# Optimization experiments

Hardware: AMD Instinct MI355X
Metric: run time of the kernel (lower is better)

## Reference

```python
import jax, jax.numpy as jnp
import numpy as np

B, T, E, H, L, V = 4, 1024, 768, 12, 6, 32000
HS = E // H
FF = 4 * E


def setup_inputs() -> dict:
    key = jax.random.key(0)
    ks = jax.random.split(key, 12)
    std = 0.02
    n = lambda k, shp: jax.random.normal(k, shp, jnp.float32) * std
    # sinusoidal position table (buffer, matches _get_pos_embed_table)
    pos = np.arange(T)[:, None].astype(np.float32)
    div = np.exp(np.arange(0, E, 2).astype(np.float32) * (-np.log(10000.0) / E))
    pet = np.zeros((T, E), np.float32)
    pet[:, 0::2] = np.sin(pos * div)
    pet[:, 1::2] = np.cos(pos * div)
    return {
        'tokens': jax.random.randint(ks[0], (B, T), 0, V),
        'targets': jax.random.randint(ks[1], (B, T), 0, V),
        'tok_emb': n(ks[2], (V, E)),
        'pet': jnp.asarray(pet),
        'wq': n(ks[3], (L, H, E, HS)),
        'wk': n(ks[4], (L, H, E, HS)),
        'wv': n(ks[5], (L, H, E, HS)),
        'w_proj': n(ks[6], (L, E, E)),
        'b_proj': jnp.zeros((L, E), jnp.float32),
        'ln1_g': jnp.ones((L, E), jnp.float32),
        'ln1_b': jnp.zeros((L, E), jnp.float32),
        'ln2_g': jnp.ones((L, E), jnp.float32),
        'ln2_b': jnp.zeros((L, E), jnp.float32),
        'w_ff1': n(ks[7], (L, E, FF)),
        'b_ff1': jnp.zeros((L, FF), jnp.float32),
        'w_ff2': n(ks[8], (L, FF, E)),
        'b_ff2': jnp.zeros((L, E), jnp.float32),
        'lnf_g': jnp.ones((E,), jnp.float32),
        'lnf_b': jnp.zeros((E,), jnp.float32),
        'w_out': n(ks[9], (E, V)),
        'b_out': jnp.zeros((V,), jnp.float32),
    }


def _ln(x, g, b, eps=1e-5):
    m = x.mean(-1, keepdims=True)
    v = ((x - m) ** 2).mean(-1, keepdims=True)
    return (x - m) / jnp.sqrt(v + eps) * g + b


def reference(tokens, targets, tok_emb, pet, wq, wk, wv, w_proj, b_proj,
              ln1_g, ln1_b, ln2_g, ln2_b, w_ff1, b_ff1, w_ff2, b_ff2,
              lnf_g, lnf_b, w_out, b_out):
    Tq = tokens.shape[1]
    x = tok_emb[tokens] + pet[:Tq]  # [B,T,E] (dropout=0 -> identity)
    mask = jnp.tril(jnp.ones((Tq, Tq), bool))
    for l in range(L):
        h = _ln(x, ln1_g[l], ln1_b[l])
        q = jnp.einsum('bte,hef->bhtf', h, wq[l])
        k = jnp.einsum('bte,hef->bhtf', h, wk[l])
        v = jnp.einsum('bte,hef->bhtf', h, wv[l])
        s = jnp.einsum('bhtf,bhsf->bhts', q, k) * (HS ** -0.5)
        s = jnp.where(mask, s, -jnp.inf)
        w = jax.nn.softmax(s, axis=-1)
        att = jnp.einsum('bhts,bhsf->bhtf', w, v)
        att = att.transpose(0, 2, 1, 3).reshape(x.shape[0], Tq, E)  # concat heads
        x = x + att @ w_proj[l] + b_proj[l]
        h2 = _ln(x, ln2_g[l], ln2_b[l])
        x = x + jax.nn.relu(h2 @ w_ff1[l] + b_ff1[l]) @ w_ff2[l] + b_ff2[l]
    x = _ln(x, lnf_g, lnf_b)
    logits = (x @ w_out + b_out).reshape(-1, V)  # [B*T, V]
    logp = jax.nn.log_softmax(logits, axis=-1)
    tgt = targets.reshape(-1)
    loss = -jnp.take_along_axis(logp, tgt[:, None], axis=1).mean()
    return logits, loss
```

## Files before the change

kernel.cpp:

```cpp
#include <hip/hip_runtime.h>
#include <math.h>

namespace {

constexpr int Bc = 4, Tc = 1024, Ec = 768, Hc = 12, Lc = 6;
constexpr int Vc = 32000, FFc = 3072, Mc = Bc * Tc;
constexpr int QKVN = 3 * Ec;

typedef __bf16 bf16x8 __attribute__((ext_vector_type(8)));
typedef float f32x4 __attribute__((ext_vector_type(4)));

__device__ __forceinline__ unsigned short f2bf(float f) {
  unsigned u = __builtin_bit_cast(unsigned, f);
  u += 0x7FFFu + ((u >> 16) & 1u);
  return (unsigned short)(u >> 16);
}

__device__ __forceinline__ float wave_sum(float v) {
#pragma unroll
  for (int off = 32; off > 0; off >>= 1) v += __shfl_xor(v, off, 64);
  return v;
}
__device__ __forceinline__ float block_sum256(float v, volatile float* red) {
  v = wave_sum(v);
  __syncthreads();
  if ((threadIdx.x & 63) == 0) red[threadIdx.x >> 6] = v;
  __syncthreads();
  return red[0] + red[1] + red[2] + red[3];
}
__device__ __forceinline__ void raw_barrier() {
  asm volatile("" ::: "memory");
  __builtin_amdgcn_s_barrier();
  asm volatile("" ::: "memory");
}

__global__ __launch_bounds__(256) void embed_k(const int* __restrict__ tokens,
                                               const float* __restrict__ emb,
                                               const float* __restrict__ pet,
                                               float* __restrict__ x) {
  int i = blockIdx.x * 256 + threadIdx.x;
  int m = i / Ec, e = i - m * Ec;
  int tok = tokens[m];
  x[i] = emb[(size_t)tok * Ec + e] + pet[(size_t)(m & (Tc - 1)) * Ec + e];
}

__global__ __launch_bounds__(256) void ln_k(const float* __restrict__ in,
                                            const float* __restrict__ g,
                                            const float* __restrict__ bb,
                                            unsigned short* __restrict__ outp) {
  __shared__ float red[4];
  int row = blockIdx.x, tid = threadIdx.x;
  const float* xr = in + (size_t)row * Ec;
  float v0 = xr[tid], v1 = xr[tid + 256], v2 = xr[tid + 512];
  float mean = block_sum256(v0 + v1 + v2, red) * (1.0f / 768.0f);
  float d0 = v0 - mean, d1 = v1 - mean, d2 = v2 - mean;
  float var = block_sum256(d0 * d0 + d1 * d1 + d2 * d2, red) * (1.0f / 768.0f);
  float rs = rsqrtf(var + 1e-5f);
  unsigned short* orow = outp + (size_t)row * Ec;
  orow[tid]       = f2bf(d0 * rs * g[tid]       + bb[tid]);
  orow[tid + 256] = f2bf(d1 * rs * g[tid + 256] + bb[tid + 256]);
  orow[tid + 512] = f2bf(d2 * rs * g[tid + 512] + bb[tid + 512]);
}

__global__ __launch_bounds__(256) void tcvt_k(const float* __restrict__ src,
                                              unsigned short* __restrict__ dst,
                                              int K, int N,
                                              size_t srcBatch, size_t dstBatch) {
  __shared__ float t[64][65];
  const float* s = src + blockIdx.z * srcBatch;
  unsigned short* d = dst + blockIdx.z * dstBatch;
  int k0 = blockIdx.y * 64, n0 = blockIdx.x * 64;
  int tid = threadIdx.x;
#pragma unroll
  for (int i = 0; i < 16; ++i) {
    int rr = (tid >> 6) + i * 4, cc = tid & 63;
    t[rr][cc] = s[(size_t)(k0 + rr) * N + n0 + cc];
  }
  __syncthreads();
#pragma unroll
  for (int i = 0; i < 16; ++i) {
    int rr = (tid >> 6) + i * 4, cc = tid & 63;
    d[(size_t)(n0 + rr) * K + k0 + cc] = f2bf(t[cc][rr]);
  }
}

__global__ __launch_bounds__(256) void qcvt_k(const float* __restrict__ wq,
                                              const float* __restrict__ wk,
                                              const float* __restrict__ wv,
                                              unsigned short* __restrict__ dst) {
  __shared__ float t[64][65];
  const int which = blockIdx.y / (Lc * Hc);
  const int z = blockIdx.y % (Lc * Hc), l = z / Hc, h = z % Hc;
  const float* src = which == 0 ? wq : (which == 1 ? wk : wv);
  const int k0 = blockIdx.x * 64;
  const int tid = threadIdx.x;
  const float* s = src + ((size_t)z * Ec + k0) * 64;
  unsigned short* d =
      dst + (size_t)l * QKVN * Ec + ((size_t)which * Ec + h * 64) * Ec + k0;
#pragma unroll
  for (int i = 0; i < 16; ++i) {
    int rr = (tid >> 6) + i * 4, cc = tid & 63;
    t[rr][cc] = s[(size_t)rr * 64 + cc];
  }
  __syncthreads();
#pragma unroll
  for (int i = 0; i < 16; ++i) {
    int rr = (tid >> 6) + i * 4, cc = tid & 63;
    d[(size_t)rr * Ec + cc] = f2bf(t[cc][rr]);
  }
}

#define GLDS16(g, l)                                              \
  __builtin_amdgcn_global_load_lds(                               \
      (const __attribute__((address_space(1))) void*)(g),         \
      (__attribute__((address_space(3))) void*)(l), 16, 0, 0)

template <int MODE, int BSRC, int BM, int BN, int GX>
__global__ __launch_bounds__(256) void mgemm_k(
    const unsigned short* __restrict__ A, const void* __restrict__ Bv,
    const float* __restrict__ bias, void* __restrict__ Cv,
    int M, int N, int K) {
  constexpr int MI = BM / 32, NF = BN / 32;
  constexpr int TL = BM / 32 + BN / 32;
  __shared__ unsigned short AsU[2][BM * 64];
  __shared__ unsigned short BsU[2][BN * 64];
  const int tid = threadIdx.x, lane = tid & 63, wave = tid >> 6;
  int bm, bn;
  if constexpr (GX == 1) {
    bm = blockIdx.y * BM;
    bn = blockIdx.x * BN;
  } else {
    bm = (blockIdx.z * GX + blockIdx.x) * BM;
    bn = blockIdx.y * BN;
  }
  const int wm = (wave >> 1) * (BM / 2), wn = (wave & 1) * (BN / 2);
  const int fr = lane & 15, fq = lane >> 4;
  const int lr8 = lane >> 3, lc8 = (lane & 7) * 8;
  const int sc8 = ((lane & 7) ^ (lr8 & 7)) * 8;
  f32x4 acc[MI][NF];
#pragma unroll
  for (int i = 0; i < MI; ++i)
#pragma unroll
    for (int j = 0; j < NF; ++j) acc[i][j] = (f32x4){0.f, 0.f, 0.f, 0.f};

  auto stage = [&](int k0, int pb) {
    {
      const unsigned short* g =
          A + (size_t)(bm + wave * (BM / 4) + lr8) * K + k0 + sc8;
      unsigned short* l = &AsU[pb][(wave * (BM / 4) + lr8) * 64 + lc8];
#pragma unroll
      for (int it = 0; it < BM / 32; ++it)
        GLDS16(g + (size_t)(it * 8) * K, l + it * 8 * 64);
    }
    if constexpr (BSRC == 0) {
      const unsigned short* Bt = (const unsigned short*)Bv;
      const unsigned short* g =
          Bt + (size_t)(bn + wave * (BN / 4) + lr8) * K + k0 + sc8;
      unsigned short* l = &BsU[pb][(wave * (BN / 4) + lr8) * 64 + lc8];
#pragma unroll
      for (int it = 0; it < BN / 32; ++it)
        GLDS16(g + (size_t)(it * 8) * K, l + it * 8 * 64);
    } else {
      const float* Bf = (const float*)Bv;
#pragma unroll
      for (int i = 0; i < 8; ++i) {
        int f4 = i * 256 + tid;
        int kk = f4 >> 5, c4 = (f4 & 31) * 4;
        float4 v = *(const float4*)(Bf + (size_t)(k0 + kk) * N + bn + c4);
        BsU[pb][(c4 + 0) * 64 + kk] = f2bf(v.x);
        BsU[pb][(c4 + 1) * 64 + kk] = f2bf(v.y);
        BsU[pb][(c4 + 2) * 64 + kk] = f2bf(v.z);
        BsU[pb][(c4 + 3) * 64 + kk] = f2bf(v.w);
      }
    }
  };

  auto compute = [&](int pb) {
#pragma unroll
    for (int kk = 0; kk < 2; ++kk) {
      bf16x8 af[MI], bfr[NF];
#pragma unroll
      for (int i = 0; i < MI; ++i) {
        int row = wm + i * 16 + fr;
        af[i] = *(const bf16x8*)((char*)AsU[pb] + row * 128 +
                                 ((kk * 64 + fq * 16) ^ ((row & 7) << 4)));
      }
#pragma unroll
      for (int j = 0; j < NF; ++j) {
        int row = wn + j * 16 + fr;
        if constexpr (BSRC == 0)
          bfr[j] = *(const bf16x8*)((char*)BsU[pb] + row * 128 +
                                    ((kk * 64 + fq * 16) ^ ((row & 7) << 4)));
        else
          bfr[j] = *(const bf16x8*)&BsU[pb][row * 64 + kk * 32 + fq * 8];
      }
#pragma unroll
      for (int i = 0; i < MI; ++i)
#pragma unroll
        for (int j = 0; j < NF; ++j)
          acc[i][j] = __builtin_amdgcn_mfma_f32_16x16x32_bf16(af[i], bfr[j],
                                                              acc[i][j], 0, 0, 0);
    }
  };

  const int nk = K >> 6;
  if constexpr (BSRC == 0) {
    stage(0, 0);
    for (int t = 0; t < nk; ++t) {
      const int pb = t & 1;
      if (t + 1 < nk) {
        stage((t + 1) << 6, pb ^ 1);
        if constexpr (TL == 8)      asm volatile("s_waitcnt vmcnt(8)" ::: "memory");
        else if constexpr (TL == 6) asm volatile("s_waitcnt vmcnt(6)" ::: "memory");
        else                        asm volatile("s_waitcnt vmcnt(4)" ::: "memory");
      } else {
        asm volatile("s_waitcnt vmcnt(0)" ::: "memory");
      }
      raw_barrier();
      compute(pb);
      raw_barrier();
    }
  } else {
    stage(0, 0);
    __syncthreads();
    for (int t = 0; t < nk; ++t) {
      const int pb = t & 1;
      if (t + 1 < nk) stage((t + 1) << 6, pb ^ 1);
      compute(pb);
      __syncthreads();
    }
  }
#pragma unroll
  for (int i = 0; i < MI; ++i) {
    int row0 = bm + wm + i * 16 + fq * 4;
#pragma unroll
    for (int j = 0; j < NF; ++j) {
      int col = bn + wn + j * 16 + fr;
      float bval = 0.f;
      if constexpr (MODE != 0) bval = bias[col];
#pragma unroll
      for (int r = 0; r < 4; ++r) {
        size_t idx = (size_t)(row0 + r) * N + col;
        float v = acc[i][j][r];
        if constexpr (MODE == 0) {
          ((unsigned short*)Cv)[idx] = f2bf(v);
        } else if constexpr (MODE == 1) {
          ((unsigned short*)Cv)[idx] = f2bf(fmaxf(v + bval, 0.f));
        } else if constexpr (MODE == 2) {
          float* C = (float*)Cv;
          C[idx] = C[idx] + v + bval;
        } else {
          ((float*)Cv)[idx] = v + bval;
        }
      }
    }
  }
}

__global__ __launch_bounds__(256) void fattn2_k(const unsigned short* __restrict__ qkv,
                                                unsigned short* __restrict__ att) {
  __shared__ unsigned short Ks[2][64 * 64];
  __shared__ unsigned short Vt[2][80 * 64];
  __shared__ unsigned short Pb[4][16 * 72];
  const int bh = blockIdx.y;
  const int b = bh / Hc, h = bh % Hc;
  const int qb = gridDim.x - 1 - blockIdx.x;
  const int q0 = qb * 128;
  const int tid = threadIdx.x, lane = tid & 63, w = tid >> 6;
  const int fr = lane & 15, fq = lane >> 4;
  const size_t base = (size_t)b * Tc * QKVN + h * 64;
  const int r0 = tid >> 3, c0 = (tid & 7) * 8;
  const int s2 = (tid & 31) * 2, c0v = (tid >> 5) * 8;
  const float SC = 0.125f * 1.44269504f;

  bf16x8 aq[2][2];
#pragma unroll
  for (int mi = 0; mi < 2; ++mi) {
    const unsigned short* qp =
        qkv + base + (size_t)(q0 + w * 32 + mi * 16 + fr) * QKVN + fq * 8;
    aq[mi][0] = *(const bf16x8*)qp;
    aq[mi][1] = *(const bf16x8*)(qp + 32);
  }
  f32x4 o[2][5];
  float m_run[2][4];
#pragma unroll
  for (int mi = 0; mi < 2; ++mi)
#pragma unroll
    for (int n = 0; n < 5; ++n) o[mi][n] = (f32x4){0.f, 0.f, 0.f, 0.f};
#pragma unroll
  for (int mi = 0; mi < 2; ++mi)
#pragma unroll
    for (int r = 0; r < 4; ++r) m_run[mi][r] = -INFINITY;

  {
#pragma unroll
    for (int bx = 0; bx < 2; ++bx) {
      unsigned* vt32 = (unsigned*)(Vt[bx] + 64 * 64);
      vt32[tid] = (tid < 32) ? 0x3F803F80u : 0u;
      vt32[tid + 256] = 0u;
    }
  }

  const int nt = 2 * qb + 2;
  uint4 pk0, pk1, pv0, pv1;
  auto loadt = [&](int s0) {
    const unsigned short* kg = qkv + base + Ec + (size_t)(s0 + r0) * QKVN + c0;
    pk0 = *(const uint4*)kg;
    pk1 = *(const uint4*)(kg + (size_t)32 * QKVN);
    const unsigned short* vg =
        qkv + base + 2 * Ec + (size_t)(s0 + s2) * QKVN + c0v;
    pv0 = *(const uint4*)vg;
    pv1 = *(const uint4*)(vg + QKVN);
  };
  auto writet = [&](int bx) {
    *(uint4*)((char*)Ks[bx] + (r0 * 128 + ((c0 * 2) ^ ((r0 & 7) << 4)))) = pk0;
    const int r1 = r0 + 32;
    *(uint4*)((char*)Ks[bx] + (r1 * 128 + ((c0 * 2) ^ ((r1 & 7) << 4)))) = pk1;
    const unsigned short* p0 = (const unsigned short*)&pv0;
    const unsigned short* p1 = (const unsigned short*)&pv1;
#pragma unroll
    for (int j = 0; j < 8; ++j) {
      int hs = c0v + j;
      unsigned pk = (unsigned)p0[j] | ((unsigned)p1[j] << 16);
      *(unsigned*)((char*)Vt[bx] + (hs * 128 + ((s2 * 2) ^ ((hs & 7) << 4)))) = pk;
    }
  };

  loadt(0);
  writet(0);
  __syncthreads();

  for (int it = 0; it < nt; ++it) {
    const int s0 = it * 64;
    const int pb = it & 1;
    if (it + 1 < nt) loadt(s0 + 64);

    f32x4 s[2][4];
#pragma unroll
    for (int mi = 0; mi < 2; ++mi)
#pragma unroll
      for (int n = 0; n < 4; ++n) s[mi][n] = (f32x4){0.f, 0.f, 0.f, 0.f};
    __builtin_amdgcn_s_setprio(1);
#pragma unroll
    for (int ss = 0; ss < 2; ++ss)
#pragma unroll
      for (int n = 0; n < 4; ++n) {
        int row = n * 16 + fr;
        bf16x8 kb = *(const bf16x8*)(
            (char*)Ks[pb] + (row * 128 + ((ss * 64 + fq * 16) ^ ((row & 7) << 4))));
#pragma unroll
        for (int mi = 0; mi < 2; ++mi)
          s[mi][n] = __builtin_amdgcn_mfma_f32_16x16x32_bf16(aq[mi][ss], kb,
                                                             s[mi][n], 0, 0, 0);
      }
    __builtin_amdgcn_s_setprio(0);

#pragma unroll
    for (int mi = 0; mi < 2; ++mi) {
      const int qlo = q0 + w * 32 + mi * 16;
      const bool need_mask = (s0 + 63 > qlo);
#pragma unroll
      for (int n = 0; n < 4; ++n) {
        int scol = s0 + n * 16 + fr;
#pragma unroll
        for (int r = 0; r < 4; ++r) {
          float v = s[mi][n][r] * SC;
          if (need_mask && scol > qlo + fq * 4 + r) v = -INFINITY;
          s[mi][n][r] = v;
        }
      }
      float mt[4];
#pragma unroll
      for (int r = 0; r < 4; ++r)
        mt[r] = fmaxf(fmaxf(s[mi][0][r], s[mi][1][r]),
                      fmaxf(s[mi][2][r], s[mi][3][r]));
#pragma unroll
      for (int off = 1; off <= 8; off <<= 1)
#pragma unroll
        for (int r = 0; r < 4; ++r)
          mt[r] = fmaxf(mt[r], __shfl_xor(mt[r], off, 64));
      bool csm = (mt[0] <= m_run[mi][0] + 8.f) & (mt[1] <= m_run[mi][1] + 8.f) &
                 (mt[2] <= m_run[mi][2] + 8.f) & (mt[3] <= m_run[mi][3] + 8.f);
      if (!__all(csm)) {
        float alpha[4];
#pragma unroll
        for (int r = 0; r < 4; ++r) {
          float mn = fmaxf(m_run[mi][r], mt[r]);
          alpha[r] = exp2f(m_run[mi][r] - mn);
          m_run[mi][r] = mn;
        }
#pragma unroll
        for (int n = 0; n < 5; ++n)
#pragma unroll
          for (int r = 0; r < 4; ++r) o[mi][n][r] *= alpha[r];
      }
#pragma unroll
      for (int n = 0; n < 4; ++n)
#pragma unroll
        for (int r = 0; r < 4; ++r)
          Pb[w][(fq * 4 + r) * 72 + n * 16 + fr] =
              f2bf(exp2f(s[mi][n][r] - m_run[mi][r]));
      __builtin_amdgcn_s_setprio(1);
#pragma unroll
      for (int ss = 0; ss < 2; ++ss) {
        bf16x8 pa = *(const bf16x8*)&Pb[w][fr * 72 + ss * 32 + fq * 8];
#pragma unroll
        for (int n = 0; n < 5; ++n) {
          int row = n * 16 + fr;
          bf16x8 vb = *(const bf16x8*)(
              (char*)Vt[pb] + (row * 128 + ((ss * 64 + fq * 16) ^ ((row & 7) << 4))));
          o[mi][n] = __builtin_amdgcn_mfma_f32_16x16x32_bf16(pa, vb, o[mi][n],
                                                             0, 0, 0);
        }
      }
      __builtin_amdgcn_s_setprio(0);
    }

    if (it + 1 < nt) writet(pb ^ 1);
    __syncthreads();
  }
#pragma unroll
  for (int mi = 0; mi < 2; ++mi)
#pragma unroll
    for (int r = 0; r < 4; ++r) {
      const float l = __shfl(o[mi][4][r], lane & 48, 64);
      const float inv = 1.0f / l;
      const int qrow = q0 + w * 32 + mi * 16 + fq * 4 + r;
      unsigned short* orow = att + ((size_t)(b * Tc + qrow)) * Ec + h * 64;
#pragma unroll
      for (int n = 0; n < 4; ++n) orow[n * 16 + fr] = f2bf(o[mi][n][r] * inv);
    }
}

__global__ __launch_bounds__(256) void loss_k(const float* __restrict__ logits,
                                              const int* __restrict__ targets,
                                              float* __restrict__ rowloss) {
  __shared__ float redm[4], reds[4];
  const int row = blockIdx.x, tid = threadIdx.x;
  const f32x4* lr4 = (const f32x4*)(logits + (size_t)row * Vc);
  float m = -INFINITY, s = 0.f;
  for (int j = tid; j < Vc / 4; j += 256) {
    f32x4 v = __builtin_nontemporal_load(lr4 + j);
    float m0 = fmaxf(fmaxf(v[0], v[1]), fmaxf(v[2], v[3]));
    float nm = fmaxf(m, m0);
    s = s * __expf(m - nm) + __expf(v[0] - nm) + __expf(v[1] - nm) +
        __expf(v[2] - nm) + __expf(v[3] - nm);
    m = nm;
  }
#pragma unroll
  for (int off = 32; off; off >>= 1) {
    float om = __shfl_xor(m, off, 64), os = __shfl_xor(s, off, 64);
    float nm = fmaxf(m, om);
    s = s * __expf(m - nm) + os * __expf(om - nm);
    m = nm;
  }
  if ((tid & 63) == 0) { redm[tid >> 6] = m; reds[tid >> 6] = s; }
  __syncthreads();
  if (tid == 0) {
    float M2 = redm[0], S2 = reds[0];
#pragma unroll
    for (int w = 1; w < 4; ++w) {
      float om = redm[w], os = reds[w];
      float nm = fmaxf(M2, om);
      S2 = S2 * __expf(M2 - nm) + os * __expf(om - nm);
      M2 = nm;
    }
    float lt = logits[(size_t)row * Vc + targets[row]];
    rowloss[row] = -(lt - M2 - logf(S2));
  }
}

__global__ __launch_bounds__(1024) void lossred_k(const float* __restrict__ rowloss,
                                                  float* __restrict__ outp) {
  __shared__ float red[16];
  float s = 0.f;
  for (int i = threadIdx.x; i < Mc; i += 1024) s += rowloss[i];
  s = wave_sum(s);
  if ((threadIdx.x & 63) == 0) red[threadIdx.x >> 6] = s;
  __syncthreads();
  if (threadIdx.x == 0) {
    float tot = 0.f;
#pragma unroll
    for (int i = 0; i < 16; ++i) tot += red[i];
    outp[0] = tot * (1.0f / (float)Mc);
  }
}

}

extern "C" void kernel_launch(void* const* d_in, const int* in_sizes, int n_in,
                              void* d_out, int out_size, void* d_ws, size_t ws_size,
                              hipStream_t stream) {
  const int*   tokens  = (const int*)d_in[0];
  const int*   targets = (const int*)d_in[1];
  const float* tok_emb = (const float*)d_in[2];
  const float* pet     = (const float*)d_in[3];
  const float* wq      = (const float*)d_in[4];
  const float* wk      = (const float*)d_in[5];
  const float* wv      = (const float*)d_in[6];
  const float* w_proj  = (const float*)d_in[7];
  const float* b_proj  = (const float*)d_in[8];
  const float* ln1_g   = (const float*)d_in[9];
  const float* ln1_b   = (const float*)d_in[10];
  const float* ln2_g   = (const float*)d_in[11];
  const float* ln2_b   = (const float*)d_in[12];
  const float* w_ff1   = (const float*)d_in[13];
  const float* b_ff1   = (const float*)d_in[14];
  const float* w_ff2   = (const float*)d_in[15];
  const float* b_ff2   = (const float*)d_in[16];
  const float* lnf_g   = (const float*)d_in[17];
  const float* lnf_b   = (const float*)d_in[18];
  const float* w_out   = (const float*)d_in[19];
  const float* b_out   = (const float*)d_in[20];

  float* out = (float*)d_out;
  char* ob = (char*)d_out;
  unsigned short* qkvA  = (unsigned short*)(ob + 0);
  unsigned short* attA  = (unsigned short*)(ob + 18874368);
  unsigned short* ffhA  = (unsigned short*)(ob + 25165824);
  unsigned short* qkvT  = (unsigned short*)(ob + 50331648);
  unsigned short* projT = (unsigned short*)(ob + 71565312);
  unsigned short* ff1T  = (unsigned short*)(ob + 78643200);
  unsigned short* ff2T  = (unsigned short*)(ob + 106954752);
  char* wb = (char*)d_ws;
  float* x = (float*)wb;
  unsigned short* hbuf = (unsigned short*)(wb + 12582912);
  float* rowloss = (float*)(wb + 18874368);
  unsigned short* woutT = (unsigned short*)(wb + 18890752);
  const bool wfit = ws_size >= (size_t)18890752 + 49152000;

  qcvt_k<<<dim3(12, 3 * Lc * Hc), 256, 0, stream>>>(wq, wk, wv, qkvT);
  tcvt_k<<<dim3(12, 12, 6), 256, 0, stream>>>(w_proj, projT, 768, 768,
                                              (size_t)589824, (size_t)589824);
  tcvt_k<<<dim3(48, 12, 6), 256, 0, stream>>>(w_ff1, ff1T, 768, 3072,
                                              (size_t)768 * 3072, (size_t)768 * 3072);
  tcvt_k<<<dim3(12, 48, 6), 256, 0, stream>>>(w_ff2, ff2T, 3072, 768,
                                              (size_t)768 * 3072, (size_t)768 * 3072);
  if (wfit)
    tcvt_k<<<dim3(500, 12, 1), 256, 0, stream>>>(w_out, woutT, 768, 32000, 0, 0);

  embed_k<<<(Mc * Ec) / 256, 256, 0, stream>>>(tokens, tok_emb, pet, x);

  for (int l = 0; l < Lc; ++l) {
    ln_k<<<Mc, 256, 0, stream>>>(x, ln1_g + (size_t)l * Ec, ln1_b + (size_t)l * Ec, hbuf);
    mgemm_k<0, 0, 128, 64, 1><<<dim3(36, 32), 256, 0, stream>>>(
        hbuf, qkvT + (size_t)l * QKVN * Ec, nullptr, qkvA, Mc, QKVN, Ec);
    fattn2_k<<<dim3(Tc / 128, Bc * Hc), 256, 0, stream>>>(qkvA, attA);
    mgemm_k<2, 0, 64, 64, 1><<<dim3(12, 64), 256, 0, stream>>>(
        attA, projT + (size_t)l * Ec * Ec, b_proj + (size_t)l * Ec, x, Mc, Ec, Ec);
    ln_k<<<Mc, 256, 0, stream>>>(x, ln2_g + (size_t)l * Ec, ln2_b + (size_t)l * Ec, hbuf);
    mgemm_k<1, 0, 128, 64, 1><<<dim3(48, 32), 256, 0, stream>>>(
        hbuf, ff1T + (size_t)l * Ec * FFc, b_ff1 + (size_t)l * FFc, ffhA, Mc, FFc, Ec);
    mgemm_k<2, 0, 64, 64, 1><<<dim3(12, 64), 256, 0, stream>>>(
        ffhA, ff2T + (size_t)l * Ec * FFc, b_ff2 + (size_t)l * Ec, x, Mc, Ec, FFc);
  }
  ln_k<<<Mc, 256, 0, stream>>>(x, lnf_g, lnf_b, hbuf);
  if (wfit)
    mgemm_k<3, 0, 128, 128, 32><<<dim3(32, 250, 1), 256, 0, stream>>>(
        hbuf, woutT, b_out, out, Mc, Vc, Ec);
  else
    mgemm_k<3, 1, 128, 128, 1><<<dim3(250, 32), 256, 0, stream>>>(
        hbuf, w_out, b_out, out, Mc, Vc, Ec);
  loss_k<<<Mc, 256, 0, stream>>>(out, targets, rowloss);
  lossred_k<<<1, 1024, 0, stream>>>(rowloss, out + (size_t)Mc * Vc);
}
```

Measured before the change: 1.711 ms.

## Fuse partial log-softmax stats into output GEMM epilogue; skip max reduction in attention

The vocab GEMM epilogue now computes per-row, per-128-column partial max and sum-exp values and writes them to a workspace buffer. A small finalize kernel merges these partials and reads the target logit, so the separate pass that re-read the full 4096x32000 fp32 logits is no longer needed. In flash attention, the per-row max shuffle reduction is now skipped when every score is within the threshold of the running max. The cost is extra epilogue work and shared-memory traffic in the GEMM, and the fused path runs only when the workspace is large enough to hold the partials.

```diff
diff --git a/kernel.cpp b/kernel.cpp
--- a/kernel.cpp
+++ b/kernel.cpp
@@ -27,6 +27,10 @@
   if ((threadIdx.x & 63) == 0) red[threadIdx.x >> 6] = v;
   __syncthreads();
   return red[0] + red[1] + red[2] + red[3];
+}
+__device__ __forceinline__ void omerge(float& m, float& s, float om, float os) {
+  if (om > m) { s = s * __expf(m - om) + os; m = om; }
+  else        { s = s + os * __expf(om - m); }
 }
 __device__ __forceinline__ void raw_barrier() {
   asm volatile("" ::: "memory");
@@ -119,7 +123,7 @@
 __global__ __launch_bounds__(256) void mgemm_k(
     const unsigned short* __restrict__ A, const void* __restrict__ Bv,
     const float* __restrict__ bias, void* __restrict__ Cv,
-    int M, int N, int K) {
+    int M, int N, int K, float* __restrict__ pbuf) {
   constexpr int MI = BM / 32, NF = BN / 32;
   constexpr int TL = BM / 32 + BN / 32;
   __shared__ unsigned short AsU[2][BM * 64];
@@ -229,6 +233,63 @@
       compute(pb);
       __syncthreads();
     }
+  }
+  if constexpr (MODE == 4) {
+    float* pms = (float*)AsU;
+    float* C = (float*)Cv;
+    float pm_[MI][4], ps_[MI][4];
+#pragma unroll
+    for (int i = 0; i < MI; ++i) {
+      int row0 = bm + wm + i * 16 + fq * 4;
+#pragma unroll
+      for (int r = 0; r < 4; ++r) {
+        float vj[NF];
+#pragma unroll
+        for (int j = 0; j < NF; ++j) {
+          int col = bn + wn + j * 16 + fr;
+          float v = acc[i][j][r] + bias[col];
+          C[(size_t)(row0 + r) * N + col] = v;
+          vj[j] = v;
+        }
+        float m = vj[0];
+#pragma unroll
+        for (int j = 1; j < NF; ++j) m = fmaxf(m, vj[j]);
+        float s = 0.f;
+#pragma unroll
+        for (int j = 0; j < NF; ++j) s += __expf(vj[j] - m);
+        pm_[i][r] = m;
+        ps_[i][r] = s;
+      }
+    }
+#pragma unroll
+    for (int off = 1; off <= 8; off <<= 1)
+#pragma unroll
+      for (int i = 0; i < MI; ++i)
+#pragma unroll
+        for (int r = 0; r < 4; ++r) {
+          float om = __shfl_xor(pm_[i][r], off, 64);
+          float os = __shfl_xor(ps_[i][r], off, 64);
+          omerge(pm_[i][r], ps_[i][r], om, os);
+        }
+    if (fr == 0) {
+#pragma unroll
+      for (int i = 0; i < MI; ++i)
+#pragma unroll
+        for (int r = 0; r < 4; ++r) {
+          int lrow = wm + i * 16 + fq * 4 + r;
+          pms[lrow * 4 + (wave & 1) * 2 + 0] = pm_[i][r];
+          pms[lrow * 4 + (wave & 1) * 2 + 1] = ps_[i][r];
+        }
+    }
+    __syncthreads();
+    if (tid < BM) {
+      float m = pms[tid * 4 + 0], s = pms[tid * 4 + 1];
+      omerge(m, s, pms[tid * 4 + 2], pms[tid * 4 + 3]);
+      size_t pi = ((size_t)(bm + tid) * (N >> 7) + (bn >> 7)) * 2;
+      pbuf[pi] = m;
+      pbuf[pi + 1] = s;
+    }
+    return;
   }
 #pragma unroll
   for (int i = 0; i < MI; ++i) {
@@ -369,19 +430,23 @@
           s[mi][n][r] = v;
         }
       }
-      float mt[4];
-#pragma unroll
-      for (int r = 0; r < 4; ++r)
-        mt[r] = fmaxf(fmaxf(s[mi][0][r], s[mi][1][r]),
-                      fmaxf(s[mi][2][r], s[mi][3][r]));
-#pragma unroll
-      for (int off = 1; off <= 8; off <<= 1)
+      bool ok = true;
+#pragma unroll
+      for (int n = 0; n < 4; ++n)
 #pragma unroll
         for (int r = 0; r < 4; ++r)
-          mt[r] = fmaxf(mt[r], __shfl_xor(mt[r], off, 64));
-      bool csm = (mt[0] <= m_run[mi][0] + 8.f) & (mt[1] <= m_run[mi][1] + 8.f) &
-                 (mt[2] <= m_run[mi][2] + 8.f) & (mt[3] <= m_run[mi][3] + 8.f);
-      if (!__all(csm)) {
+          ok &= (s[mi][n][r] <= m_run[mi][r] + 8.f);
+      if (!__all(ok)) {
+        float mt[4];
+#pragma unroll
+        for (int r = 0; r < 4; ++r)
+          mt[r] = fmaxf(fmaxf(s[mi][0][r], s[mi][1][r]),
+                        fmaxf(s[mi][2][r], s[mi][3][r]));
+#pragma unroll
+        for (int off = 1; off <= 8; off <<= 1)
+#pragma unroll
+          for (int r = 0; r < 4; ++r)
+            mt[r] = fmaxf(mt[r], __shfl_xor(mt[r], off, 64));
         float alpha[4];
 #pragma unroll
         for (int r = 0; r < 4; ++r) {
@@ -430,6 +495,26 @@
 #pragma unroll
       for (int n = 0; n < 4; ++n) orow[n * 16 + fr] = f2bf(o[mi][n][r] * inv);
     }
+}
+
+__global__ __launch_bounds__(256) void lossfin_k(const float* __restrict__ pbuf,
+                                                 const float* __restrict__ logits,
+                                                 const int* __restrict__ targets,
+                                                 float* __restrict__ rowloss) {
+  const int row = blockIdx.x * 4 + (threadIdx.x >> 6);
+  const int lane = threadIdx.x & 63;
+  const float* p = pbuf + (size_t)row * 500;
+  float m = -INFINITY, s = 0.f;
+  for (int j = lane; j < 250; j += 64) omerge(m, s, p[j * 2], p[j * 2 + 1]);
+#pragma unroll
+  for (int off = 32; off > 0; off >>= 1) {
+    float om = __shfl_xor(m, off, 64), os = __shfl_xor(s, off, 64);
+    omerge(m, s, om, os);
+  }
+  if (lane == 0) {
+    float lt = logits[(size_t)row * Vc + targets[row]];
+    rowloss[row] = -(lt - m - logf(s));
+  }
 }
 
 __global__ __launch_bounds__(256) void loss_k(const float* __restrict__ logits,
@@ -527,7 +612,9 @@
   unsigned short* hbuf = (unsigned short*)(wb + 12582912);
   float* rowloss = (float*)(wb + 18874368);
   unsigned short* woutT = (unsigned short*)(wb + 18890752);
+  float* pbuf = (float*)(wb + 68042752);
   const bool wfit = ws_size >= (size_t)18890752 + 49152000;
+  const bool pfit = ws_size >= (size_t)68042752 + 8192000;
 
   qcvt_k<<<dim3(12, 3 * Lc * Hc), 256, 0, stream>>>(wq, wk, wv, qkvT);
   tcvt_k<<<dim3(12, 12, 6), 256, 0, stream>>>(w_proj, projT, 768, 768,
@@ -544,23 +631,29 @@
   for (int l = 0; l < Lc; ++l) {
     ln_k<<<Mc, 256, 0, stream>>>(x, ln1_g + (size_t)l * Ec, ln1_b + (size_t)l * Ec, hbuf);
     mgemm_k<0, 0, 128, 64, 1><<<dim3(36, 32), 256, 0, stream>>>(
-        hbuf, qkvT + (size_t)l * QKVN * Ec, nullptr, qkvA, Mc, QKVN, Ec);
+        hbuf, qkvT + (size_t)l * QKVN * Ec, nullptr, qkvA, Mc, QKVN, Ec, nullptr);
     fattn2_k<<<dim3(Tc / 128, Bc * Hc), 256, 0, stream>>>(qkvA, attA);
     mgemm_k<2, 0, 64, 64, 1><<<dim3(12, 64), 256, 0, stream>>>(
-        attA, projT + (size_t)l * Ec * Ec, b_proj + (size_t)l * Ec, x, Mc, Ec, Ec);
+        attA, projT + (size_t)l * Ec * Ec, b_proj + (size_t)l * Ec, x, Mc, Ec, Ec, nullptr);
     ln_k<<<Mc, 256, 0, stream>>>(x, ln2_g + (size_t)l * Ec, ln2_b + (size_t)l * Ec, hbuf);
     mgemm_k<1, 0, 128, 64, 1><<<dim3(48, 32), 256, 0, stream>>>(
-        hbuf, ff1T + (size_t)l * Ec * FFc, b_ff1 + (size_t)l * FFc, ffhA, Mc, FFc, Ec);
+        hbuf, ff1T + (size_t)l * Ec * FFc, b_ff1 + (size_t)l * FFc, ffhA, Mc, FFc, Ec, nullptr);
     mgemm_k<2, 0, 64, 64, 1><<<dim3(12, 64), 256, 0, stream>>>(
-        ffhA, ff2T + (size_t)l * Ec * FFc, b_ff2 + (size_t)l * Ec, x, Mc, Ec, FFc);
+        ffhA, ff2T + (size_t)l * Ec * FFc, b_ff2 + (size_t)l * Ec, x, Mc, Ec, FFc, nullptr);
   }
   ln_k<<<Mc, 256, 0, stream>>>(x, lnf_g, lnf_b, hbuf);
-  if (wfit)
+  if (wfit && pfit) {
+    mgemm_k<4, 0, 128, 128, 32><<<dim3(32, 250, 1), 256, 0, stream>>>(
+        hbuf, woutT, b_out, out, Mc, Vc, Ec, pbuf);
+    lossfin_k<<<Mc / 4, 256, 0, stream>>>(pbuf, out, targets, rowloss);
+  } else if (wfit) {
     mgemm_k<3, 0, 128, 128, 32><<<dim3(32, 250, 1), 256, 0, stream>>>(
-        hbuf, woutT, b_out, out, Mc, Vc, Ec);
-  else
+        hbuf, woutT, b_out, out, Mc, Vc, Ec, nullptr);
+    loss_k<<<Mc, 256, 0, stream>>>(out, targets, rowloss);
+  } else {
     mgemm_k<3, 1, 128, 128, 1><<<dim3(250, 32), 256, 0, stream>>>(
-        hbuf, w_out, b_out, out, Mc, Vc, Ec);
-  loss_k<<<Mc, 256, 0, stream>>>(out, targets, rowloss);
+        hbuf, w_out, b_out, out, Mc, Vc, Ec, nullptr);
+    loss_k<<<Mc, 256, 0, stream>>>(out, targets, rowloss);
+  }
   lossred_k<<<1, 1024, 0, stream>>>(rowloss, out + (size_t)Mc * Vc);
 }
```

New measurement: 1.713 ms. No clear change (+0.1%).
